# Kernel tuning notes

Hardware: AMD Instinct MI355X
Metric: run time of the kernel (lower is better)

Reference implementation:

```python
import jax, jax.numpy as jnp
import numpy as np

# Module config (matches init_kwargs)
G, K, S = 64, 3, 2          # base patch size, num scales, scale factor
B, H, W, C = 64, 512, 512, 3
HG, HL = 128, 128
D_IN = K * G * G * C


def setup_inputs() -> dict:
    key = jax.random.key(0)
    kx, kl, k1, k2 = jax.random.split(key, 4)
    x = jax.random.normal(kx, (B, H, W, C), dtype=jnp.float32)
    # glimpse locations in [-1, 1)
    l = jax.random.uniform(kl, (B, 2), minval=-1.0, maxval=1.0, dtype=jnp.float32)
    # fc1: phi (D_IN -> HG); fc2: l (2 -> HL). PyTorch-Linear-like scale.
    W1 = jax.random.normal(k1, (D_IN, HG), dtype=jnp.float32) / np.sqrt(D_IN)
    b1 = jnp.zeros((HG,), dtype=jnp.float32)
    W2 = jax.random.normal(k2, (2, HL), dtype=jnp.float32) / np.sqrt(2.0)
    b2 = jnp.zeros((HL,), dtype=jnp.float32)
    return {"x": x, "l": l, "W1": W1, "b1": b1, "W2": W2, "b2": b2}


def _extract_glimpse(x, l):
    """Retina: k multi-scale patches centered at l, resized to (G,G).
    Returns (B, K, G, G, C)."""
    sizes = [G * S**i for i in range(K)]              # 64, 128, 256
    pad = sizes[-1] // 2 + 1                          # pad once for largest scale
    xp = jnp.pad(x, ((0, 0), (pad, pad), (pad, pad), (0, 0)))
    # denormalize: [-1,1] -> [0,H], truncated to int (torch .long())
    coords = (0.5 * (l + 1.0) * H).astype(jnp.int32)  # (B,2): col0=x, col1=y
    patches = []
    for size in sizes:
        fy = coords[:, 1] - size // 2 + pad
        fx = coords[:, 0] - size // 2 + pad

        def slice_one(img, y0, x0, size=size):
            return jax.lax.dynamic_slice(img, (y0, x0, 0), (size, size, C))

        p = jax.vmap(slice_one)(xp, fy, fx)           # (B, size, size, C)
        f = size // G
        if f > 1:  # downsample by integer factor via average pooling
            p = p.reshape(B, G, f, G, f, C).mean(axis=(2, 4))
        patches.append(p)
    return jnp.stack(patches, axis=1)                 # (B, K, G, G, C)


def reference(x, l, W1, b1, W2, b2):
    phi = _extract_glimpse(x, l).reshape(x.shape[0], -1)   # (B, K*G*G*C)
    phi_out = jax.nn.relu(phi @ W1 + b1)                   # (B, HG)
    l_out = jax.nn.relu(l @ W2 + b2)                       # (B, HL)
    return jax.nn.relu(jnp.concatenate([phi_out, l_out], axis=1))
```

## Files before the change

kernel.cpp:

```cpp
#include <hip/hip_runtime.h>

#define G_     64
#define NK     3
#define NB     64
#define IH     512
#define IW     512
#define NC     3
#define HG_    128
#define HL_    128
#define D_IN_    (NK * G_ * G_ * NC)
#define D_SCALE  (G_ * G_ * NC)
#define KCH      128
#define NCHUNK   (D_IN_ / KCH)
#define BSPLIT   4
#define NBLK     (NCHUNK * BSPLIT)
#define PSTRIDE  (NB * HG_)

template <int F>
__device__ __forceinline__ void scale_body(
    const float* __restrict__ x, const float* __restrict__ l,
    const float* __restrict__ W1, float* __restrict__ P,
    int roff, int d0, int b0, int chunkGlobal,
    float (&phi_s)[16][KCH], float (&red2)[16][HG_], int* cx_s, int* cy_s)
{
    const int tid = threadIdx.x;
    if (tid < 16) {
        float lx = l[(b0 + tid) * 2 + 0];
        float ly = l[(b0 + tid) * 2 + 1];
        cx_s[tid] = (int)((0.5f * (lx + 1.0f)) * 512.0f);
        cy_s[tid] = (int)((0.5f * (ly + 1.0f)) * 512.0f);
    }
    __syncthreads();

    const int dd   = tid & (KCH - 1);
    const int jb0  = (tid >> 7) * 8;
    const int r    = roff + dd;
    const int gy   = r / (G_ * NC);
    const int rem  = r - gy * (G_ * NC);
    const int gx   = rem / NC;
    const int c    = rem - gx * NC;
    constexpr float inv = 1.0f / (float)(F * F);
    constexpr int JU = (F == 4) ? 2 : 8;

#pragma unroll 1
    for (int jo = 0; jo < 8; jo += JU) {
        float sums[JU];
#pragma unroll
        for (int ji = 0; ji < JU; ++ji) {
            const int jb = jb0 + jo + ji;
            const int b  = b0 + jb;
            const int by = cy_s[jb] - 32 * F + gy * F;
            const int bx = cx_s[jb] - 32 * F + gx * F;
            const float* bimg = x + (size_t)b * (IH * IW * NC) + c;
            float s = 0.0f;
#pragma unroll
            for (int dy = 0; dy < F; ++dy) {
                const int y = by + dy;
                const bool yok = (unsigned)y < (unsigned)IH;
#pragma unroll
                for (int dx = 0; dx < F; ++dx) {
                    const int xx = bx + dx;
                    const bool ok = yok && ((unsigned)xx < (unsigned)IW);
                    s += ok ? bimg[(size_t)y * (IW * NC) + xx * NC] : 0.0f;
                }
            }
            sums[ji] = s;
        }
#pragma unroll
        for (int ji = 0; ji < JU; ++ji)
            phi_s[jb0 + jo + ji][dd] = sums[ji] * inv;
    }
    __syncthreads();

    const int hq  = tid & 31;
    const int h0  = hq * 4;
    const int gg  = tid >> 5;
    const int bg4 = (gg & 3) * 4;
    const int dh  = gg >> 2;
    const int db  = dh * 64;

    float4 a0 = {0.f, 0.f, 0.f, 0.f};
    float4 a1 = {0.f, 0.f, 0.f, 0.f};
    float4 a2 = {0.f, 0.f, 0.f, 0.f};
    float4 a3 = {0.f, 0.f, 0.f, 0.f};
    const float* wp = W1 + (size_t)(d0 + db) * HG_ + h0;

#pragma unroll 2
    for (int t = 0; t < 16; ++t) {
        const float4 pv0 = *(const float4*)&phi_s[bg4 + 0][db + 4 * t];
        const float4 pv1 = *(const float4*)&phi_s[bg4 + 1][db + 4 * t];
        const float4 pv2 = *(const float4*)&phi_s[bg4 + 2][db + 4 * t];
        const float4 pv3 = *(const float4*)&phi_s[bg4 + 3][db + 4 * t];
#pragma unroll
        for (int u = 0; u < 4; ++u) {
            const float4 wv = *(const float4*)(wp + (size_t)(4 * t + u) * HG_);
            const float p0 = (&pv0.x)[u];
            const float p1 = (&pv1.x)[u];
            const float p2 = (&pv2.x)[u];
            const float p3 = (&pv3.x)[u];
            a0.x = fmaf(p0, wv.x, a0.x); a0.y = fmaf(p0, wv.y, a0.y);
            a0.z = fmaf(p0, wv.z, a0.z); a0.w = fmaf(p0, wv.w, a0.w);
            a1.x = fmaf(p1, wv.x, a1.x); a1.y = fmaf(p1, wv.y, a1.y);
            a1.z = fmaf(p1, wv.z, a1.z); a1.w = fmaf(p1, wv.w, a1.w);
            a2.x = fmaf(p2, wv.x, a2.x); a2.y = fmaf(p2, wv.y, a2.y);
            a2.z = fmaf(p2, wv.z, a2.z); a2.w = fmaf(p2, wv.w, a2.w);
            a3.x = fmaf(p3, wv.x, a3.x); a3.y = fmaf(p3, wv.y, a3.y);
            a3.z = fmaf(p3, wv.z, a3.z); a3.w = fmaf(p3, wv.w, a3.w);
        }
    }

    if (dh == 1) {
        *(float4*)&red2[bg4 + 0][h0] = a0;
        *(float4*)&red2[bg4 + 1][h0] = a1;
        *(float4*)&red2[bg4 + 2][h0] = a2;
        *(float4*)&red2[bg4 + 3][h0] = a3;
    }
    __syncthreads();
    if (dh == 0) {
        float* pb = P + (size_t)chunkGlobal * PSTRIDE + (size_t)(b0 + bg4) * HG_ + h0;
        const float4 r0 = *(const float4*)&red2[bg4 + 0][h0];
        const float4 r1 = *(const float4*)&red2[bg4 + 1][h0];
        const float4 r2 = *(const float4*)&red2[bg4 + 2][h0];
        const float4 r3 = *(const float4*)&red2[bg4 + 3][h0];
        *(float4*)(pb + 0 * HG_) =
            make_float4(a0.x + r0.x, a0.y + r0.y, a0.z + r0.z, a0.w + r0.w);
        *(float4*)(pb + 1 * HG_) =
            make_float4(a1.x + r1.x, a1.y + r1.y, a1.z + r1.z, a1.w + r1.w);
        *(float4*)(pb + 2 * HG_) =
            make_float4(a2.x + r2.x, a2.y + r2.y, a2.z + r2.z, a2.w + r2.w);
        *(float4*)(pb + 3 * HG_) =
            make_float4(a3.x + r3.x, a3.y + r3.y, a3.z + r3.z, a3.w + r3.w);
    }
}

__global__ __launch_bounds__(256) void fused(
    const float* __restrict__ x, const float* __restrict__ l,
    const float* __restrict__ W1, float* __restrict__ P)
{
    __shared__ float phi_s[16][KCH];
    __shared__ float red2[16][HG_];
    __shared__ int cx_s[16], cy_s[16];

    const int cg = blockIdx.x >> 2;
    const int b0 = (blockIdx.x & 3) * 16;

    if (cg < 96) {
        const int cl = cg;
        scale_body<4>(x, l, W1, P, cl * KCH, 2 * D_SCALE + cl * KCH, b0, cg,
                      phi_s, red2, cx_s, cy_s);
    } else if (cg < 192) {
        const int cl = cg - 96;
        scale_body<2>(x, l, W1, P, cl * KCH, D_SCALE + cl * KCH, b0, cg,
                      phi_s, red2, cx_s, cy_s);
    } else {
        const int cl = cg - 192;
        scale_body<1>(x, l, W1, P, cl * KCH, cl * KCH, b0, cg,
                      phi_s, red2, cx_s, cy_s);
    }
}

__global__ __launch_bounds__(256) void reduce_epilogue(
    const float* __restrict__ P,
    const float* __restrict__ l,
    const float* __restrict__ b1,
    const float* __restrict__ W2,
    const float* __restrict__ b2,
    float* __restrict__ out)
{
    __shared__ float4 red[32][8];
    const int b    = blockIdx.x >> 2;
    const int q    = blockIdx.x & 3;
    const int t    = threadIdx.x;
    const int lane = t & 7;
    const int grp  = t >> 3;

    const float4* p4 = (const float4*)P
                     + (size_t)(grp * 9) * (PSTRIDE / 4)
                     + (size_t)b * (HG_ / 4) + q * 8 + lane;
    float4 a = make_float4(0.f, 0.f, 0.f, 0.f);
#pragma unroll
    for (int i = 0; i < 9; ++i) {
        const float4 v = p4[(size_t)i * (PSTRIDE / 4)];
        a.x += v.x; a.y += v.y; a.z += v.z; a.w += v.w;
    }
    red[grp][lane] = a;
    __syncthreads();

#pragma unroll
    for (int s = 16; s >= 1; s >>= 1) {
        if (grp < s) {
            const float4 o = red[grp + s][lane];
            float4 m = red[grp][lane];
            m.x += o.x; m.y += o.y; m.z += o.z; m.w += o.w;
            red[grp][lane] = m;
        }
        __syncthreads();
    }

    if (t < 8) {
        const float4 a2 = red[0][t];
        const float4 bb = ((const float4*)b1)[q * 8 + t];
        float4 o;
        o.x = fmaxf(a2.x + bb.x, 0.0f);
        o.y = fmaxf(a2.y + bb.y, 0.0f);
        o.z = fmaxf(a2.z + bb.z, 0.0f);
        o.w = fmaxf(a2.w + bb.w, 0.0f);
        ((float4*)out)[(size_t)b * ((HG_ + HL_) / 4) + q * 8 + t] = o;
    } else if (t >= 64 && t < 96) {
        const int h = q * 32 + (t - 64);
        const float l0 = l[b * 2 + 0];
        const float l1 = l[b * 2 + 1];
        const float v = fmaf(l1, W2[HL_ + h], fmaf(l0, W2[h], b2[h]));
        out[(size_t)b * (HG_ + HL_) + HG_ + h] = fmaxf(v, 0.0f);
    }
}

extern "C" void kernel_launch(void* const* d_in, const int* in_sizes, int n_in,
                              void* d_out, int out_size, void* d_ws, size_t ws_size,
                              hipStream_t stream) {
    const float* x  = (const float*)d_in[0];
    const float* l  = (const float*)d_in[1];
    const float* W1 = (const float*)d_in[2];
    const float* b1 = (const float*)d_in[3];
    const float* W2 = (const float*)d_in[4];
    const float* b2 = (const float*)d_in[5];
    float* out = (float*)d_out;
    float* P = (float*)d_ws;

    fused<<<NBLK, 256, 0, stream>>>(x, l, W1, P);
    reduce_epilogue<<<NB * 4, 256, 0, stream>>>(P, l, b1, W2, b2, out);
}
```

Baseline: 277.7 us.

## Split batch into 8-sample blocks and 4-way K-split within GEMV tiles

Each block now handles 8 batch rows instead of 16, doubling the grid, and the in-block matmul splits the 128-wide K chunk four ways instead of two, with a three-buffer shared reduction. It also asks for 8 waves-per-SIMD occupancy through launch bounds. The aim is more parallelism and occupancy for the latency-bound gather. In exchange each W1 chunk is reread by twice as many blocks, and the launch-bounds hint may force register spilling.

```diff
diff --git a/kernel.cpp b/kernel.cpp
--- a/kernel.cpp
+++ b/kernel.cpp
@@ -12,7 +12,7 @@
 #define D_SCALE  (G_ * G_ * NC)
 #define KCH      128
 #define NCHUNK   (D_IN_ / KCH)
-#define BSPLIT   4
+#define BSPLIT   8
 #define NBLK     (NCHUNK * BSPLIT)
 #define PSTRIDE  (NB * HG_)
 
@@ -21,10 +21,10 @@
     const float* __restrict__ x, const float* __restrict__ l,
     const float* __restrict__ W1, float* __restrict__ P,
     int roff, int d0, int b0, int chunkGlobal,
-    float (&phi_s)[16][KCH], float (&red2)[16][HG_], int* cx_s, int* cy_s)
+    float (&phi_s)[8][KCH], float (&red2)[3][8][HG_], int* cx_s, int* cy_s)
 {
     const int tid = threadIdx.x;
-    if (tid < 16) {
+    if (tid < 8) {
         float lx = l[(b0 + tid) * 2 + 0];
         float ly = l[(b0 + tid) * 2 + 1];
         cx_s[tid] = (int)((0.5f * (lx + 1.0f)) * 512.0f);
@@ -33,17 +33,17 @@
     __syncthreads();
 
     const int dd   = tid & (KCH - 1);
-    const int jb0  = (tid >> 7) * 8;
+    const int jb0  = (tid >> 7) * 4;
     const int r    = roff + dd;
     const int gy   = r / (G_ * NC);
     const int rem  = r - gy * (G_ * NC);
     const int gx   = rem / NC;
     const int c    = rem - gx * NC;
     constexpr float inv = 1.0f / (float)(F * F);
-    constexpr int JU = (F == 4) ? 2 : 8;
+    constexpr int JU = (F == 4) ? 2 : 4;
 
 #pragma unroll 1
-    for (int jo = 0; jo < 8; jo += JU) {
+    for (int jo = 0; jo < 4; jo += JU) {
         float sums[JU];
 #pragma unroll
         for (int ji = 0; ji < JU; ++ji) {
@@ -75,9 +75,9 @@
     const int hq  = tid & 31;
     const int h0  = hq * 4;
     const int gg  = tid >> 5;
-    const int bg4 = (gg & 3) * 4;
-    const int dh  = gg >> 2;
-    const int db  = dh * 64;
+    const int bg4 = (gg & 1) * 4;
+    const int dq  = gg >> 1;
+    const int db  = dq * 32;
 
     float4 a0 = {0.f, 0.f, 0.f, 0.f};
     float4 a1 = {0.f, 0.f, 0.f, 0.f};
@@ -85,8 +85,8 @@
     float4 a3 = {0.f, 0.f, 0.f, 0.f};
     const float* wp = W1 + (size_t)(d0 + db) * HG_ + h0;
 
-#pragma unroll 2
-    for (int t = 0; t < 16; ++t) {
+#pragma unroll 1
+    for (int t = 0; t < 8; ++t) {
         const float4 pv0 = *(const float4*)&phi_s[bg4 + 0][db + 4 * t];
         const float4 pv1 = *(const float4*)&phi_s[bg4 + 1][db + 4 * t];
         const float4 pv2 = *(const float4*)&phi_s[bg4 + 2][db + 4 * t];
@@ -109,40 +109,43 @@
         }
     }
 
-    if (dh == 1) {
-        *(float4*)&red2[bg4 + 0][h0] = a0;
-        *(float4*)&red2[bg4 + 1][h0] = a1;
-        *(float4*)&red2[bg4 + 2][h0] = a2;
-        *(float4*)&red2[bg4 + 3][h0] = a3;
-    }
-    __syncthreads();
-    if (dh == 0) {
+    if (dq != 0) {
+        *(float4*)&red2[dq - 1][bg4 + 0][h0] = a0;
+        *(float4*)&red2[dq - 1][bg4 + 1][h0] = a1;
+        *(float4*)&red2[dq - 1][bg4 + 2][h0] = a2;
+        *(float4*)&red2[dq - 1][bg4 + 3][h0] = a3;
+    }
+    __syncthreads();
+    if (dq == 0) {
         float* pb = P + (size_t)chunkGlobal * PSTRIDE + (size_t)(b0 + bg4) * HG_ + h0;
-        const float4 r0 = *(const float4*)&red2[bg4 + 0][h0];
-        const float4 r1 = *(const float4*)&red2[bg4 + 1][h0];
-        const float4 r2 = *(const float4*)&red2[bg4 + 2][h0];
-        const float4 r3 = *(const float4*)&red2[bg4 + 3][h0];
-        *(float4*)(pb + 0 * HG_) =
-            make_float4(a0.x + r0.x, a0.y + r0.y, a0.z + r0.z, a0.w + r0.w);
-        *(float4*)(pb + 1 * HG_) =
-            make_float4(a1.x + r1.x, a1.y + r1.y, a1.z + r1.z, a1.w + r1.w);
-        *(float4*)(pb + 2 * HG_) =
-            make_float4(a2.x + r2.x, a2.y + r2.y, a2.z + r2.z, a2.w + r2.w);
-        *(float4*)(pb + 3 * HG_) =
-            make_float4(a3.x + r3.x, a3.y + r3.y, a3.z + r3.z, a3.w + r3.w);
-    }
-}
-
-__global__ __launch_bounds__(256) void fused(
+#pragma unroll
+        for (int q = 0; q < 3; ++q) {
+            const float4 r0 = *(const float4*)&red2[q][bg4 + 0][h0];
+            const float4 r1 = *(const float4*)&red2[q][bg4 + 1][h0];
+            const float4 r2 = *(const float4*)&red2[q][bg4 + 2][h0];
+            const float4 r3 = *(const float4*)&red2[q][bg4 + 3][h0];
+            a0.x += r0.x; a0.y += r0.y; a0.z += r0.z; a0.w += r0.w;
+            a1.x += r1.x; a1.y += r1.y; a1.z += r1.z; a1.w += r1.w;
+            a2.x += r2.x; a2.y += r2.y; a2.z += r2.z; a2.w += r2.w;
+            a3.x += r3.x; a3.y += r3.y; a3.z += r3.z; a3.w += r3.w;
+        }
+        *(float4*)(pb + 0 * HG_) = a0;
+        *(float4*)(pb + 1 * HG_) = a1;
+        *(float4*)(pb + 2 * HG_) = a2;
+        *(float4*)(pb + 3 * HG_) = a3;
+    }
+}
+
+__global__ __launch_bounds__(256, 8) void fused(
     const float* __restrict__ x, const float* __restrict__ l,
     const float* __restrict__ W1, float* __restrict__ P)
 {
-    __shared__ float phi_s[16][KCH];
-    __shared__ float red2[16][HG_];
-    __shared__ int cx_s[16], cy_s[16];
-
-    const int cg = blockIdx.x >> 2;
-    const int b0 = (blockIdx.x & 3) * 16;
+    __shared__ float phi_s[8][KCH];
+    __shared__ float red2[3][8][HG_];
+    __shared__ int cx_s[8], cy_s[8];
+
+    const int cg = blockIdx.x >> 3;
+    const int b0 = (blockIdx.x & 7) * 8;
 
     if (cg < 96) {
         const int cl = cg;
```

After: 279.6 us. No clear change (+0.7%).
